# Optimization experiments

Hardware: AMD Instinct MI355X
Metric: run time of the kernel (lower is better)

The kernel has to match this reference:

```python
import jax, jax.numpy as jnp
import numpy as np

N_NODES = 200000
N_EDGES = 500000
N_RELS = 256
D = 256  # rnn_in_dim == rnn_hid_dim


def setup_inputs() -> dict:
    key = jax.random.key(0)
    ks = jax.random.split(key, 8)
    src_nid = jax.random.randint(ks[0], (N_EDGES,), 0, N_NODES, dtype=jnp.int32)
    dst_nid = jax.random.randint(ks[1], (N_EDGES,), 0, N_NODES, dtype=jnp.int32)
    rel = jax.random.randint(ks[2], (N_EDGES,), 0, N_RELS, dtype=jnp.int32)
    static_entity_emb = jax.random.normal(ks[3], (N_NODES, D), dtype=jnp.float32)
    dynamic_relation_emb = jax.random.normal(ks[4], (N_RELS, 1, D, 2), dtype=jnp.float32)
    s = 1.0 / np.sqrt(D)
    W_ih = jax.random.uniform(ks[5], (3 * D, D), jnp.float32, -s, s)
    W_hh = jax.random.uniform(ks[6], (3 * D, D), jnp.float32, -s, s)
    kb1, kb2 = jax.random.split(ks[7])
    b_ih = jax.random.uniform(kb1, (3 * D,), jnp.float32, -s, s)
    b_hh = jax.random.uniform(kb2, (3 * D,), jnp.float32, -s, s)
    return {"src_nid": src_nid, "dst_nid": dst_nid, "rel": rel,
            "static_entity_emb": static_entity_emb,
            "dynamic_relation_emb": dynamic_relation_emb,
            "W_ih": W_ih, "W_hh": W_hh, "b_ih": b_ih, "b_hh": b_hh}


def _segment_mean(x, ids, num_segments):
    # x: [E, D], ids: [E] -> [R, D] mean per relation (0 where empty, as scatter_mean)
    sums = jax.ops.segment_sum(x, ids, num_segments=num_segments)
    cnts = jax.ops.segment_sum(jnp.ones((ids.shape[0],), x.dtype), ids,
                               num_segments=num_segments)
    return sums / jnp.maximum(cnts, 1.0)[:, None]


def _gru_cell(x, h, W_ih, W_hh, b_ih, b_hh):
    # PyTorch GRU cell, single step. x,h: [R, H]
    gi = x @ W_ih.T + b_ih            # [R, 3H]
    gh = h @ W_hh.T + b_hh            # [R, 3H]
    i_r, i_z, i_n = jnp.split(gi, 3, axis=-1)
    h_r, h_z, h_n = jnp.split(gh, 3, axis=-1)
    r = jax.nn.sigmoid(i_r + h_r)
    z = jax.nn.sigmoid(i_z + h_z)
    n = jnp.tanh(i_n + r * h_n)
    return (1.0 - z) * n + z * h


def reference(src_nid, dst_nid, rel, static_entity_emb, dynamic_relation_emb,
              W_ih, W_hh, b_ih, b_hh):
    R = dynamic_relation_emb.shape[0]
    # gather node embeddings by edge endpoints, mean-reduce per relation
    src_avg = _segment_mean(static_entity_emb[src_nid], rel, R)  # [R, D]
    dst_avg = _segment_mean(static_entity_emb[dst_nid], rel, R)  # [R, D]
    h_src = dynamic_relation_emb[:, 0, :, 0]  # num_layers==1 -> [R, H]
    h_dst = dynamic_relation_emb[:, 0, :, 1]
    new_src = _gru_cell(src_avg, h_src, W_ih, W_hh, b_ih, b_hh)
    new_dst = _gru_cell(dst_avg, h_dst, W_ih, W_hh, b_ih, b_hh)
    # [R, num_layers=1, H, 2]
    return jnp.stack([new_src, new_dst], axis=-1)[:, None, :, :]
```

## Files before the change

kernel.cpp:

```cpp
#include <hip/hip_runtime.h>
#include <math.h>

#define D 256
#define R 256
#define DIMC 64

__device__ __forceinline__ float sigmoidf(float x) {
    return 1.0f / (1.0f + expf(-x));
}

__global__ void zero_ws(float* ws, int n) {
    int i = blockIdx.x * blockDim.x + threadIdx.x;
    if (i < n) ws[i] = 0.0f;
}

__global__ __launch_bounds__(256) void hist_kernel(const int* __restrict__ rel,
                                                   int E,
                                                   float* __restrict__ counts) {
    __shared__ int h[R];
    h[threadIdx.x] = 0;
    __syncthreads();
    for (int e = blockIdx.x * blockDim.x + threadIdx.x; e < E;
         e += gridDim.x * blockDim.x)
        atomicAdd(&h[rel[e]], 1);
    __syncthreads();
    atomicAdd(&counts[threadIdx.x], (float)h[threadIdx.x]);
}

__global__ __launch_bounds__(1024, 8) void scatter_kernel(
    const int* __restrict__ src_nid, const int* __restrict__ dst_nid,
    const int* __restrict__ rel, const float* __restrict__ emb,
    float* __restrict__ src_sum, float* __restrict__ dst_sum, int E, int epb) {
    __shared__ float acc[R * DIMC];
    const int tid = threadIdx.x;
    for (int i = tid; i < R * DIMC; i += 1024) acc[i] = 0.0f;
    __syncthreads();

    const int* nids = blockIdx.z ? dst_nid : src_nid;
    float* gsum     = blockIdx.z ? dst_sum : src_sum;
    const int dimbase = blockIdx.y * DIMC;
    const int lane = tid & 63;
    const int wave = tid >> 6;
    const int start = blockIdx.x * epb;
    const int end   = (start + epb < E) ? (start + epb) : E;
    const int dl = dimbase + lane;

    for (int base = start + wave * 64; base < end; base += 1024) {
        int rem = end - base;
        int cnt = rem < 64 ? rem : 64;
        int mynid = 0, myrel = 0;
        if (lane < cnt) {
            mynid = nids[base + lane];
            myrel = rel[base + lane];
        }
        int i = 0;
        for (; i + 16 <= cnt; i += 16) {
            float v[16];
#pragma unroll
            for (int j = 0; j < 16; j++) {
                int n = __builtin_amdgcn_readlane(mynid, i + j);
                v[j] = emb[(size_t)n * D + dl];
            }
#pragma unroll
            for (int j = 0; j < 16; j++) {
                int rr = __builtin_amdgcn_readlane(myrel, i + j);
                atomicAdd(&acc[rr * DIMC + lane], v[j]);
            }
        }
        for (; i < cnt; i++) {
            int n  = __builtin_amdgcn_readlane(mynid, i);
            int rr = __builtin_amdgcn_readlane(myrel, i);
            float v = emb[(size_t)n * D + dl];
            atomicAdd(&acc[rr * DIMC + lane], v);
        }
    }
    __syncthreads();
    for (int i = tid; i < R * DIMC; i += 1024) {
        int r = i >> 6;
        int d = i & 63;
        atomicAdd(&gsum[r * D + dimbase + d], acc[i]);
    }
}

__global__ __launch_bounds__(256) void gru_kernel(
    const float* __restrict__ src_sum, const float* __restrict__ dst_sum,
    const float* __restrict__ counts, const float* __restrict__ dyn,
    const float* __restrict__ W_ih, const float* __restrict__ W_hh,
    const float* __restrict__ b_ih, const float* __restrict__ b_hh,
    float* __restrict__ out) {
    __shared__ float xs[D], xd[D], hs[D], hd[D];
    const int r = blockIdx.x, t = threadIdx.x;
    float inv = 1.0f / fmaxf(counts[r], 1.0f);
    xs[t] = src_sum[r * D + t] * inv;
    xd[t] = dst_sum[r * D + t] * inv;
    float h_s = dyn[(r * D + t) * 2 + 0];
    float h_d = dyn[(r * D + t) * 2 + 1];
    hs[t] = h_s;
    hd[t] = h_d;
    __syncthreads();

    float gis[3], gid[3], ghs[3], ghd[3];
#pragma unroll
    for (int g = 0; g < 3; g++) {
        int row = g * D + t;
        const float4* wi = (const float4*)(W_ih + (size_t)row * D);
        const float4* wh = (const float4*)(W_hh + (size_t)row * D);
        float ais = 0.f, aid = 0.f, ahs = 0.f, ahd = 0.f;
        for (int k = 0; k < D / 4; k++) {
            float4 a = wi[k];
            float4 b = wh[k];
            int k4 = k * 4;
            ais += a.x * xs[k4] + a.y * xs[k4 + 1] + a.z * xs[k4 + 2] + a.w * xs[k4 + 3];
            aid += a.x * xd[k4] + a.y * xd[k4 + 1] + a.z * xd[k4 + 2] + a.w * xd[k4 + 3];
            ahs += b.x * hs[k4] + b.y * hs[k4 + 1] + b.z * hs[k4 + 2] + b.w * hs[k4 + 3];
            ahd += b.x * hd[k4] + b.y * hd[k4 + 1] + b.z * hd[k4 + 2] + b.w * hd[k4 + 3];
        }
        float bi = b_ih[row];
        float bh = b_hh[row];
        gis[g] = ais + bi; gid[g] = aid + bi;
        ghs[g] = ahs + bh; ghd[g] = ahd + bh;
    }
    float rs = sigmoidf(gis[0] + ghs[0]);
    float zs = sigmoidf(gis[1] + ghs[1]);
    float ns = tanhf(gis[2] + rs * ghs[2]);
    float new_s = (1.0f - zs) * ns + zs * h_s;

    float rd = sigmoidf(gid[0] + ghd[0]);
    float zd = sigmoidf(gid[1] + ghd[1]);
    float nd = tanhf(gid[2] + rd * ghd[2]);
    float new_d = (1.0f - zd) * nd + zd * h_d;

    out[(r * D + t) * 2 + 0] = new_s;
    out[(r * D + t) * 2 + 1] = new_d;
}

extern "C" void kernel_launch(void* const* d_in, const int* in_sizes, int n_in,
                              void* d_out, int out_size, void* d_ws, size_t ws_size,
                              hipStream_t stream) {
    const int* src_nid = (const int*)d_in[0];
    const int* dst_nid = (const int*)d_in[1];
    const int* rel     = (const int*)d_in[2];
    const float* emb   = (const float*)d_in[3];
    const float* dyn   = (const float*)d_in[4];
    const float* W_ih  = (const float*)d_in[5];
    const float* W_hh  = (const float*)d_in[6];
    const float* b_ih  = (const float*)d_in[7];
    const float* b_hh  = (const float*)d_in[8];
    float* out = (float*)d_out;
    const int E = in_sizes[0];

    float* ws      = (float*)d_ws;
    float* src_sum = ws;
    float* dst_sum = ws + R * D;
    float* counts  = ws + 2 * R * D;
    const int nzero = 2 * R * D + R;

    zero_ws<<<(nzero + 255) / 256, 256, 0, stream>>>(ws, nzero);
    hist_kernel<<<256, 256, 0, stream>>>(rel, E, counts);

    const int chunks = 64;
    const int epb = (E + chunks - 1) / chunks;
    scatter_kernel<<<dim3(chunks, 4, 2), 1024, 0, stream>>>(
        src_nid, dst_nid, rel, emb, src_sum, dst_sum, E, epb);

    gru_kernel<<<R, 256, 0, stream>>>(src_sum, dst_sum, counts, dyn, W_ih, W_hh,
                                      b_ih, b_hh, out);
}
```

Baseline: 1.550 ms.

## Switch scatter to per-lane edge gathers with swizzled LDS and split GRU directions

```diff
diff --git a/kernel.cpp b/kernel.cpp
--- a/kernel.cpp
+++ b/kernel.cpp
@@ -43,95 +43,90 @@
     const int wave = tid >> 6;
     const int start = blockIdx.x * epb;
     const int end   = (start + epb < E) ? (start + epb) : E;
-    const int dl = dimbase + lane;
 
     for (int base = start + wave * 64; base < end; base += 1024) {
-        int rem = end - base;
-        int cnt = rem < 64 ? rem : 64;
+        const int e = base + lane;
+        const bool valid = e < end;
         int mynid = 0, myrel = 0;
-        if (lane < cnt) {
-            mynid = nids[base + lane];
-            myrel = rel[base + lane];
+        if (valid) {
+            mynid = nids[e];
+            myrel = rel[e];
         }
-        int i = 0;
-        for (; i + 16 <= cnt; i += 16) {
-            float v[16];
+        const float4* row =
+            (const float4*)(emb + (size_t)mynid * D + dimbase);
 #pragma unroll
-            for (int j = 0; j < 16; j++) {
-                int n = __builtin_amdgcn_readlane(mynid, i + j);
-                v[j] = emb[(size_t)n * D + dl];
+        for (int c = 0; c < 4; c++) {
+            float4 v[4];
+#pragma unroll
+            for (int k = 0; k < 4; k++) v[k] = row[c * 4 + k];
+            if (valid) {
+#pragma unroll
+                for (int k = 0; k < 4; k++) {
+                    const int d0 = c * 16 + k * 4;
+                    atomicAdd(&acc[(d0 + 0) * R + (myrel ^ ((d0 + 0) & 31))], v[k].x);
+                    atomicAdd(&acc[(d0 + 1) * R + (myrel ^ ((d0 + 1) & 31))], v[k].y);
+                    atomicAdd(&acc[(d0 + 2) * R + (myrel ^ ((d0 + 2) & 31))], v[k].z);
+                    atomicAdd(&acc[(d0 + 3) * R + (myrel ^ ((d0 + 3) & 31))], v[k].w);
+                }
             }
-#pragma unroll
-            for (int j = 0; j < 16; j++) {
-                int rr = __builtin_amdgcn_readlane(myrel, i + j);
-                atomicAdd(&acc[rr * DIMC + lane], v[j]);
-            }
-        }
-        for (; i < cnt; i++) {
-            int n  = __builtin_amdgcn_readlane(mynid, i);
-            int rr = __builtin_amdgcn_readlane(myrel, i);
-            float v = emb[(size_t)n * D + dl];
-            atomicAdd(&acc[rr * DIMC + lane], v);
         }
     }
     __syncthreads();
     for (int i = tid; i < R * DIMC; i += 1024) {
-        int r = i >> 6;
-        int d = i & 63;
-        atomicAdd(&gsum[r * D + dimbase + d], acc[i]);
+        const int d = i & (DIMC - 1);
+        const int r = i >> 6;
+        atomicAdd(&gsum[r * D + dimbase + d], acc[d * R + (r ^ (d & 31))]);
     }
 }
 
-__global__ __launch_bounds__(256) void gru_kernel(
+__global__ __launch_bounds__(512) void gru_kernel(
     const float* __restrict__ src_sum, const float* __restrict__ dst_sum,
     const float* __restrict__ counts, const float* __restrict__ dyn,
     const float* __restrict__ W_ih, const float* __restrict__ W_hh,
     const float* __restrict__ b_ih, const float* __restrict__ b_hh,
     float* __restrict__ out) {
-    __shared__ float xs[D], xd[D], hs[D], hd[D];
+    __shared__ float x2[2][D], h2[2][D];
     const int r = blockIdx.x, t = threadIdx.x;
-    float inv = 1.0f / fmaxf(counts[r], 1.0f);
-    xs[t] = src_sum[r * D + t] * inv;
-    xd[t] = dst_sum[r * D + t] * inv;
-    float h_s = dyn[(r * D + t) * 2 + 0];
-    float h_d = dyn[(r * D + t) * 2 + 1];
-    hs[t] = h_s;
-    hd[t] = h_d;
+    const int s = t >> 8;
+    const int tt = t & 255;
+    const float inv = 1.0f / fmaxf(counts[r], 1.0f);
+    float h_old;
+    if (s == 0) {
+        x2[0][tt] = src_sum[r * D + tt] * inv;
+        h_old = dyn[(r * D + tt) * 2 + 0];
+        h2[0][tt] = h_old;
+    } else {
+        x2[1][tt] = dst_sum[r * D + tt] * inv;
+        h_old = dyn[(r * D + tt) * 2 + 1];
+        h2[1][tt] = h_old;
+    }
     __syncthreads();
+    const float* xs = x2[s];
+    const float* hs = h2[s];
 
-    float gis[3], gid[3], ghs[3], ghd[3];
+    float gi[3], gh[3];
 #pragma unroll
     for (int g = 0; g < 3; g++) {
-        int row = g * D + t;
+        const int row = g * D + tt;
         const float4* wi = (const float4*)(W_ih + (size_t)row * D);
         const float4* wh = (const float4*)(W_hh + (size_t)row * D);
-        float ais = 0.f, aid = 0.f, ahs = 0.f, ahd = 0.f;
+        float ai = 0.f, ah = 0.f;
         for (int k = 0; k < D / 4; k++) {
             float4 a = wi[k];
             float4 b = wh[k];
             int k4 = k * 4;
-            ais += a.x * xs[k4] + a.y * xs[k4 + 1] + a.z * xs[k4 + 2] + a.w * xs[k4 + 3];
-            aid += a.x * xd[k4] + a.y * xd[k4 + 1] + a.z * xd[k4 + 2] + a.w * xd[k4 + 3];
-            ahs += b.x * hs[k4] + b.y * hs[k4 + 1] + b.z * hs[k4 + 2] + b.w * hs[k4 + 3];
-            ahd += b.x * hd[k4] + b.y * hd[k4 + 1] + b.z * hd[k4 + 2] + b.w * hd[k4 + 3];
+            ai += a.x * xs[k4] + a.y * xs[k4 + 1] + a.z * xs[k4 + 2] + a.w * xs[k4 + 3];
+            ah += b.x * hs[k4] + b.y * hs[k4 + 1] + b.z * hs[k4 + 2] + b.w * hs[k4 + 3];
         }
-        float bi = b_ih[row];
-        float bh = b_hh[row];
-        gis[g] = ais + bi; gid[g] = aid + bi;
-        ghs[g] = ahs + bh; ghd[g] = ahd + bh;
+        gi[g] = ai + b_ih[row];
+        gh[g] = ah + b_hh[row];
     }
-    float rs = sigmoidf(gis[0] + ghs[0]);
-    float zs = sigmoidf(gis[1] + ghs[1]);
-    float ns = tanhf(gis[2] + rs * ghs[2]);
-    float new_s = (1.0f - zs) * ns + zs * h_s;
+    const float rr = sigmoidf(gi[0] + gh[0]);
+    const float zz = sigmoidf(gi[1] + gh[1]);
+    const float nn = tanhf(gi[2] + rr * gh[2]);
+    const float nh = (1.0f - zz) * nn + zz * h_old;
 
-    float rd = sigmoidf(gid[0] + ghd[0]);
-    float zd = sigmoidf(gid[1] + ghd[1]);
-    float nd = tanhf(gid[2] + rd * ghd[2]);
-    float new_d = (1.0f - zd) * nd + zd * h_d;
-
-    out[(r * D + t) * 2 + 0] = new_s;
-    out[(r * D + t) * 2 + 1] = new_d;
+    out[(r * D + tt) * 2 + s] = nh;
 }
 
 extern "C" void kernel_launch(void* const* d_in, const int* in_sizes, int n_in,
@@ -163,6 +158,6 @@
     scatter_kernel<<<dim3(chunks, 4, 2), 1024, 0, stream>>>(
         src_nid, dst_nid, rel, emb, src_sum, dst_sum, E, epb);
 
-    gru_kernel<<<R, 256, 0, stream>>>(src_sum, dst_sum, counts, dyn, W_ih, W_hh,
+    gru_kernel<<<R, 512, 0, stream>>>(src_sum, dst_sum, counts, dyn, W_ih, W_hh,
                                       b_ih, b_hh, out);
 }
```

Result: slower. 1.596 ms (+3.0%).
